# Optimization experiments

Measured on AMD Instinct MI355X. Metric: run time of the kernel, lower is better.

## Reference

```python
import jax, jax.numpy as jnp
import numpy as np

B, S, D = 2, 4096, 1024
H = 16
DK = D // H  # 64


def setup_inputs() -> dict:
    key = jax.random.key(0)
    ks = jax.random.split(key, 7)
    scale = 1.0 / np.sqrt(D)
    return {
        "Q": jax.random.normal(ks[0], (B, S, D), jnp.float32),
        "K": jax.random.normal(ks[1], (B, S, D), jnp.float32),
        "V": jax.random.normal(ks[2], (B, S, D), jnp.float32),
        "Wq": jax.random.normal(ks[3], (H * DK, D), jnp.float32) * scale,
        "Wk": jax.random.normal(ks[4], (H * DK, D), jnp.float32) * scale,
        "Wv": jax.random.normal(ks[5], (H * DK, D), jnp.float32) * scale,
        "Wo": jax.random.normal(ks[6], (D, H * DK), jnp.float32) * scale,
    }


def reference(Q, K, V, Wq, Wk, Wv, Wo):
    # Linear projections (bias=False): x @ W.T
    q = (Q @ Wq.T).reshape(B, S, H, DK)  # slicing [:, :, i*dk:(i+1)*dk] == head axis
    k = (K @ Wk.T).reshape(B, S, H, DK)
    v = (V @ Wv.T).reshape(B, S, H, DK)
    # scores: softmax(QK^T / sqrt(d_k)) per head, no mask
    scores = jnp.einsum("bshd,bthd->bhst", q, k) / jnp.sqrt(jnp.float32(DK))
    attn = jax.nn.softmax(scores, axis=-1)
    heads = jnp.einsum("bhst,bthd->bshd", attn, v)  # (B, S, H, DK)
    out = heads.reshape(B, S, H * DK) @ Wo.T  # concat heads then output proj
    return out
```

## Files before the change

### kernel.cpp

```cpp
#include <hip/hip_runtime.h>
#include <hip/hip_bf16.h>
#include <math.h>

#define B_NUM 2
#define S_LEN 4096
#define D_DIM 1024
#define H_NUM 16
#define DKH   64

typedef __attribute__((ext_vector_type(8))) short short8;
typedef __attribute__((ext_vector_type(4))) float f32x4;

__device__ __forceinline__ unsigned short f2bf(float f) {
    unsigned int u = __float_as_uint(f);
    u = (u + 0x7FFFu + ((u >> 16) & 1u)) >> 16;
    return (unsigned short)u;
}

__device__ __forceinline__ unsigned pk_bf16(float lo, float hi) {
    __hip_bfloat162 h = __float22bfloat162_rn(make_float2(lo, hi));
    unsigned u; __builtin_memcpy(&u, &h, 4); return u;
}

__device__ __forceinline__ void async_ld16(const unsigned short* g, unsigned short* l) {
    __builtin_amdgcn_global_load_lds(
        (const __attribute__((address_space(1))) unsigned int*)g,
        (__attribute__((address_space(3))) unsigned int*)l, 16, 0, 0);
}

__global__ __launch_bounds__(256) void f2b_3(
    const float* __restrict__ x0, const float* __restrict__ x1, const float* __restrict__ x2,
    unsigned short* __restrict__ y0, unsigned short* __restrict__ y1, unsigned short* __restrict__ y2)
{
    const float* xs[3] = { x0, x1, x2 };
    unsigned short* ys[3] = { y0, y1, y2 };
    const float* x = xs[blockIdx.y];
    unsigned short* y = ys[blockIdx.y];
    int i = (blockIdx.x * 256 + threadIdx.x) * 8;
    float4 a = *(const float4*)(x + i);
    float4 b = *(const float4*)(x + i + 4);
    unsigned t[4] = { pk_bf16(a.x, a.y), pk_bf16(a.z, a.w),
                      pk_bf16(b.x, b.y), pk_bf16(b.z, b.w) };
    *(uint4*)(y + i) = *(const uint4*)t;
}
__global__ __launch_bounds__(256) void f2b_4(
    const float* __restrict__ x0, const float* __restrict__ x1,
    const float* __restrict__ x2, const float* __restrict__ x3,
    unsigned short* __restrict__ y0, unsigned short* __restrict__ y1,
    unsigned short* __restrict__ y2, unsigned short* __restrict__ y3)
{
    const float* xs[4] = { x0, x1, x2, x3 };
    unsigned short* ys[4] = { y0, y1, y2, y3 };
    const float* x = xs[blockIdx.y];
    unsigned short* y = ys[blockIdx.y];
    int i = (blockIdx.x * 256 + threadIdx.x) * 8;
    float4 a = *(const float4*)(x + i);
    float4 b = *(const float4*)(x + i + 4);
    unsigned t[4] = { pk_bf16(a.x, a.y), pk_bf16(a.z, a.w),
                      pk_bf16(b.x, b.y), pk_bf16(b.z, b.w) };
    *(uint4*)(y + i) = *(const uint4*)t;
}

__device__ __forceinline__ void gemm_core(
    const unsigned short* __restrict__ A, const unsigned short* __restrict__ Wt,
    unsigned short* As, unsigned short* Bs,
    int m0, int n0, int K, f32x4 (&acc)[4][4])
{
    const int tid  = threadIdx.x;
    const int lane = tid & 63;
    const int wave = tid >> 6;
    const int quad = lane >> 4;
    const int l15  = lane & 15;
    const int wm = (wave >> 1) * 64;
    const int wn = (wave & 1) * 64;

    const int c0 = tid, c1 = tid + 256;
    const unsigned short* A0 = A  + (size_t)(m0 + (c0 >> 2)) * K + (c0 & 3) * 8;
    const unsigned short* A1 = A  + (size_t)(m0 + (c1 >> 2)) * K + (c1 & 3) * 8;
    const unsigned short* W0 = Wt + (size_t)(n0 + (c0 >> 2)) * K + (c0 & 3) * 8;
    const unsigned short* W1 = Wt + (size_t)(n0 + (c1 >> 2)) * K + (c1 & 3) * 8;

    for (int k0 = 0; k0 < K; k0 += 32) {
        __syncthreads();
        async_ld16(A0 + k0, &As[c0 * 8]);
        async_ld16(A1 + k0, &As[c1 * 8]);
        async_ld16(W0 + k0, &Bs[c0 * 8]);
        async_ld16(W1 + k0, &Bs[c1 * 8]);
        __syncthreads();

        short8 af[4], bfr[4];
        #pragma unroll
        for (int i = 0; i < 4; ++i)
            af[i] = *(const short8*)&As[(wm + i * 16 + l15) * 32 + quad * 8];
        #pragma unroll
        for (int j = 0; j < 4; ++j)
            bfr[j] = *(const short8*)&Bs[(wn + j * 16 + l15) * 32 + quad * 8];
        #pragma unroll
        for (int i = 0; i < 4; ++i)
            #pragma unroll
            for (int j = 0; j < 4; ++j)
                acc[i][j] = __builtin_amdgcn_mfma_f32_16x16x32_bf16(af[i], bfr[j], acc[i][j], 0, 0, 0);
    }
}

__global__ __launch_bounds__(256) void gemm_qkv(
    const unsigned short* __restrict__ Qb, const unsigned short* __restrict__ Kb,
    const unsigned short* __restrict__ Vb,
    const unsigned short* __restrict__ Wq, const unsigned short* __restrict__ Wk,
    const unsigned short* __restrict__ Wv,
    unsigned short* __restrict__ qo, unsigned short* __restrict__ ko,
    unsigned short* __restrict__ vto)
{
    __shared__ unsigned short As[128 * 32];
    __shared__ unsigned short Bs[128 * 32];

    const int z = blockIdx.z;
    const unsigned short* A  = (z == 0) ? Qb : (z == 1) ? Kb : Vb;
    const unsigned short* Wt = (z == 0) ? Wq : (z == 1) ? Wk : Wv;
    const float scale = (z == 0) ? 0.125f * 1.4426950408889634f : 1.0f;

    const int m0 = blockIdx.y * 128;
    const int n0 = blockIdx.x * 128;

    const f32x4 fzero = {0.f, 0.f, 0.f, 0.f};
    f32x4 acc[4][4];
    #pragma unroll
    for (int i = 0; i < 4; ++i)
        #pragma unroll
        for (int j = 0; j < 4; ++j) acc[i][j] = fzero;

    gemm_core(A, Wt, As, Bs, m0, n0, D_DIM, acc);

    const int lane = threadIdx.x & 63;
    const int wave = threadIdx.x >> 6;
    const int quad = lane >> 4;
    const int l15  = lane & 15;
    const int wm = (wave >> 1) * 64;
    const int wn = (wave & 1) * 64;

    if (z < 2) {
        unsigned short* out = (z == 0) ? qo : ko;
        #pragma unroll
        for (int i = 0; i < 4; ++i)
            #pragma unroll
            for (int j = 0; j < 4; ++j)
                #pragma unroll
                for (int r = 0; r < 4; ++r) {
                    const int row = m0 + wm + i * 16 + quad * 4 + r;
                    const int col = n0 + wn + j * 16 + l15;
                    out[(size_t)row * D_DIM + col] = f2bf(acc[i][j][r] * scale);
                }
    } else {
        #pragma unroll
        for (int i = 0; i < 4; ++i)
            #pragma unroll
            for (int j = 0; j < 4; ++j) {
                const int row = m0 + wm + i * 16 + quad * 4;
                const int col = n0 + wn + j * 16 + l15;
                const int bb = row >> 12, ss = row & (S_LEN - 1);
                uint2 u;
                u.x = pk_bf16(acc[i][j][0], acc[i][j][1]);
                u.y = pk_bf16(acc[i][j][2], acc[i][j][3]);
                *(uint2*)&vto[((size_t)(bb * H_NUM * DKH) + col) * S_LEN + ss] = u;
            }
    }
}

__global__ __launch_bounds__(256) void gemm_out(
    const unsigned short* __restrict__ A, const unsigned short* __restrict__ Wt,
    float* __restrict__ C)
{
    __shared__ unsigned short As[128 * 32];
    __shared__ unsigned short Bs[128 * 32];

    const int m0 = blockIdx.y * 128;
    const int n0 = blockIdx.x * 128;

    const f32x4 fzero = {0.f, 0.f, 0.f, 0.f};
    f32x4 acc[4][4];
    #pragma unroll
    for (int i = 0; i < 4; ++i)
        #pragma unroll
        for (int j = 0; j < 4; ++j) acc[i][j] = fzero;

    gemm_core(A, Wt, As, Bs, m0, n0, D_DIM, acc);

    const int lane = threadIdx.x & 63;
    const int wave = threadIdx.x >> 6;
    const int quad = lane >> 4;
    const int l15  = lane & 15;
    const int wm = (wave >> 1) * 64;
    const int wn = (wave & 1) * 64;

    #pragma unroll
    for (int i = 0; i < 4; ++i)
        #pragma unroll
        for (int j = 0; j < 4; ++j)
            #pragma unroll
            for (int r = 0; r < 4; ++r) {
                const int row = m0 + wm + i * 16 + quad * 4 + r;
                const int col = n0 + wn + j * 16 + l15;
                C[(size_t)row * D_DIM + col] = acc[i][j][r];
            }
}

__global__ __launch_bounds__(256, 2) void flash_mfma(
    const unsigned short* __restrict__ q, const unsigned short* __restrict__ k,
    const unsigned short* __restrict__ vt, unsigned short* __restrict__ hp)
{
    __shared__ unsigned short Ks[64 * 64];
    __shared__ unsigned short Vt[64 * 64];
    __shared__ unsigned short Ps[256 * 64];

    const int tid  = threadIdx.x;
    const int lane = tid & 63;
    const int wave = tid >> 6;
    const int quad = lane >> 4;
    const int l15  = lane & 15;

    const int bx   = blockIdx.x;
    const int xcd  = bx & 7, slot = bx >> 3;
    const int g    = xcd + 8 * (slot >> 4);
    const int s0   = (slot & 15) * 256;
    const int b    = g >> 4, h = g & 15;
    const size_t base = (size_t)b * (S_LEN * D_DIM) + (size_t)h * DKH;
    const size_t vtb  = (size_t)g * (DKH * S_LEN);

    short8 qf[4][2];
    #pragma unroll
    for (int nb = 0; nb < 4; ++nb)
        #pragma unroll
        for (int kk = 0; kk < 2; ++kk)
            qf[nb][kk] = *(const short8*)(q + base +
                (size_t)(s0 + wave * 64 + nb * 16 + l15) * D_DIM + kk * 32 + quad * 8);

    const f32x4 fzero = {0.f, 0.f, 0.f, 0.f};
    f32x4 o[4][4];
    float lacc[4] = {};
    #pragma unroll
    for (int i = 0; i < 4; ++i)
        #pragma unroll
        for (int j = 0; j < 4; ++j) o[i][j] = fzero;

    const int sr  = tid >> 3;
    const int sch = tid & 7;

    uint4 kpre[2], vpre[2];
    #pragma unroll
    for (int it = 0; it < 2; ++it) {
        const int r = sr + it * 32;
        kpre[it] = *(const uint4*)(k + base + (size_t)r * D_DIM + sch * 8);
        vpre[it] = *(const uint4*)(vt + vtb + (size_t)r * S_LEN + sch * 8);
    }

    for (int t0 = 0; t0 < S_LEN; t0 += 64) {
        __syncthreads();
        #pragma unroll
        for (int it = 0; it < 2; ++it) {
            const int r = sr + it * 32;
            *(uint4*)&Ks[r * 64 + ((sch ^ (r & 7)) << 3)] = kpre[it];
            *(uint4*)&Vt[r * 64 + ((sch ^ (r & 7)) << 3)] = vpre[it];
        }
        __syncthreads();
        if (t0 + 64 < S_LEN) {
            #pragma unroll
            for (int it = 0; it < 2; ++it) {
                const int r = sr + it * 32;
                kpre[it] = *(const uint4*)(k + base + (size_t)(t0 + 64 + r) * D_DIM + sch * 8);
                vpre[it] = *(const uint4*)(vt + vtb + (size_t)r * S_LEN + t0 + 64 + sch * 8);
            }
        }

        #pragma unroll
        for (int mh = 0; mh < 2; ++mh) {
            short8 kf[2][2];
            #pragma unroll
            for (int mi = 0; mi < 2; ++mi)
                #pragma unroll
                for (int kk = 0; kk < 2; ++kk) {
                    const int rr = (mh * 2 + mi) * 16 + l15;
                    kf[mi][kk] = *(const short8*)&Ks[rr * 64 + (((kk * 4 + quad) ^ (rr & 7)) << 3)];
                }
            f32x4 st[2][4];
            #pragma unroll
            for (int mi = 0; mi < 2; ++mi)
                #pragma unroll
                for (int nb = 0; nb < 4; ++nb) st[mi][nb] = fzero;
            #pragma unroll
            for (int kk = 0; kk < 2; ++kk)
                #pragma unroll
                for (int mi = 0; mi < 2; ++mi)
                    #pragma unroll
                    for (int nb = 0; nb < 4; ++nb)
                        st[mi][nb] = __builtin_amdgcn_mfma_f32_16x16x32_bf16(
                            kf[mi][kk], qf[nb][kk], st[mi][nb], 0, 0, 0);

            #pragma unroll
            for (int mi = 0; mi < 2; ++mi)
                #pragma unroll
                for (int nb = 0; nb < 4; ++nb) {
                    float p0 = __builtin_amdgcn_exp2f(st[mi][nb][0]);
                    float p1 = __builtin_amdgcn_exp2f(st[mi][nb][1]);
                    float p2 = __builtin_amdgcn_exp2f(st[mi][nb][2]);
                    float p3 = __builtin_amdgcn_exp2f(st[mi][nb][3]);
                    lacc[nb] += (p0 + p1) + (p2 + p3);
                    uint2 u;
                    u.x = pk_bf16(p0, p1);
                    u.y = pk_bf16(p2, p3);
                    const int row = wave * 64 + nb * 16 + l15;
                    const int c8  = (mh * 2 + mi) * 4 + quad;
                    *(uint2*)&Ps[row * 64 + ((c8 ^ (l15 & 14)) << 2)] = u;
                }
        }

        #pragma unroll
        for (int kk = 0; kk < 2; ++kk) {
            short8 vf[4], pf[4];
            #pragma unroll
            for (int mb = 0; mb < 4; ++mb) {
                const int rv = mb * 16 + l15;
                vf[mb] = *(const short8*)&Vt[rv * 64 + (((kk * 4 + quad) ^ (rv & 7)) << 3)];
            }
            #pragma unroll
            for (int nb = 0; nb < 4; ++nb) {
                const int rp = wave * 64 + nb * 16 + l15;
                pf[nb] = *(const short8*)&Ps[rp * 64 + (((kk * 8 + quad * 2) ^ (l15 & 14)) << 2)];
            }
            #pragma unroll
            for (int mb = 0; mb < 4; ++mb)
                #pragma unroll
                for (int nb = 0; nb < 4; ++nb)
                    o[mb][nb] = __builtin_amdgcn_mfma_f32_16x16x32_bf16(
                        vf[mb], pf[nb], o[mb][nb], 0, 0, 0);
        }
    }

    #pragma unroll
    for (int nb = 0; nb < 4; ++nb) {
        float l = lacc[nb];
        l += __shfl_xor(l, 16);
        l += __shfl_xor(l, 32);
        const float inv = 1.f / l;
        const int row = s0 + wave * 64 + nb * 16 + l15;
        #pragma unroll
        for (int mb = 0; mb < 4; ++mb) {
            uint2 u;
            u.x = pk_bf16(o[mb][nb][0] * inv, o[mb][nb][1] * inv);
            u.y = pk_bf16(o[mb][nb][2] * inv, o[mb][nb][3] * inv);
            *(uint2*)&hp[base + (size_t)row * D_DIM + mb * 16 + quad * 4] = u;
        }
    }
}

extern "C" void kernel_launch(void* const* d_in, const int* in_sizes, int n_in,
                              void* d_out, int out_size, void* d_ws, size_t ws_size,
                              hipStream_t stream) {
    const float* Q  = (const float*)d_in[0];
    const float* K  = (const float*)d_in[1];
    const float* V  = (const float*)d_in[2];
    const float* Wq = (const float*)d_in[3];
    const float* Wk = (const float*)d_in[4];
    const float* Wv = (const float*)d_in[5];
    const float* Wo = (const float*)d_in[6];

    const int NBSD = 8388608;
    const int NW   = 1048576;

    unsigned short* Qb  = (unsigned short*)d_ws;
    unsigned short* Kb  = Qb  + NBSD;
    unsigned short* Vb  = Kb  + NBSD;
    unsigned short* Wqb = Vb  + NBSD;
    unsigned short* Wkb = Wqb + NW;
    unsigned short* Wvb = Wkb + NW;
    unsigned short* Wob = Wvb + NW;
    unsigned short* qp  = Wob + NW;
    unsigned short* kp  = qp  + NBSD;
    unsigned short* vtp = kp  + NBSD;
    unsigned short* hb  = vtp + NBSD;

    f2b_3<<<dim3(NBSD / 2048, 3), 256, 0, stream>>>(Q, K, V, Qb, Kb, Vb);
    f2b_4<<<dim3(NW / 2048, 4), 256, 0, stream>>>(Wq, Wk, Wv, Wo, Wqb, Wkb, Wvb, Wob);

    const int M = B_NUM * S_LEN;
    dim3 gqkv(D_DIM / 128, M / 128, 3);
    gemm_qkv<<<gqkv, 256, 0, stream>>>(Qb, Kb, Vb, Wqb, Wkb, Wvb, qp, kp, vtp);

    flash_mfma<<<512, 256, 0, stream>>>(qp, kp, vtp, hb);

    gemm_out<<<dim3(D_DIM / 128, M / 128), 256, 0, stream>>>(hb, Wob, (float*)d_out);
}
```

Before: 464.4 us.

## Double-buffer K/V shared tiles and raise wave priority around MFMA blocks

Turns the K and Vt shared-memory tiles into two-stage ping-pong buffers. Each iteration stores the next tile into the idle buffer while computing on the current one, which cuts the two barriers per iteration to one. It also wraps the MFMA loops in s_setprio so waves issuing matrix instructions get scheduling priority over waves doing loads and exp. The cost is 16 KB of extra LDS per block, which may reduce occupancy at the requested 2 blocks per CU.

```diff
diff --git a/kernel.cpp b/kernel.cpp
--- a/kernel.cpp
+++ b/kernel.cpp
@@ -208,8 +208,8 @@
     const unsigned short* __restrict__ q, const unsigned short* __restrict__ k,
     const unsigned short* __restrict__ vt, unsigned short* __restrict__ hp)
 {
-    __shared__ unsigned short Ks[64 * 64];
-    __shared__ unsigned short Vt[64 * 64];
+    __shared__ unsigned short Ks[2][64 * 64];
+    __shared__ unsigned short Vt[2][64 * 64];
     __shared__ unsigned short Ps[256 * 64];
 
     const int tid  = threadIdx.x;
@@ -244,30 +244,43 @@
 
     const int sr  = tid >> 3;
     const int sch = tid & 7;
+    const int swz0 = ((sch ^ (sr & 7)) << 3);
+    const int swz1 = ((sch ^ ((sr + 32) & 7)) << 3);
 
     uint4 kpre[2], vpre[2];
-    #pragma unroll
-    for (int it = 0; it < 2; ++it) {
-        const int r = sr + it * 32;
-        kpre[it] = *(const uint4*)(k + base + (size_t)r * D_DIM + sch * 8);
-        vpre[it] = *(const uint4*)(vt + vtb + (size_t)r * S_LEN + sch * 8);
+    {
+        kpre[0] = *(const uint4*)(k + base + (size_t)sr * D_DIM + sch * 8);
+        kpre[1] = *(const uint4*)(k + base + (size_t)(sr + 32) * D_DIM + sch * 8);
+        vpre[0] = *(const uint4*)(vt + vtb + (size_t)sr * S_LEN + sch * 8);
+        vpre[1] = *(const uint4*)(vt + vtb + (size_t)(sr + 32) * S_LEN + sch * 8);
+        *(uint4*)&Ks[0][sr * 64 + swz0] = kpre[0];
+        *(uint4*)&Ks[0][(sr + 32) * 64 + swz1] = kpre[1];
+        *(uint4*)&Vt[0][sr * 64 + swz0] = vpre[0];
+        *(uint4*)&Vt[0][(sr + 32) * 64 + swz1] = vpre[1];
+        kpre[0] = *(const uint4*)(k + base + (size_t)(64 + sr) * D_DIM + sch * 8);
+        kpre[1] = *(const uint4*)(k + base + (size_t)(64 + sr + 32) * D_DIM + sch * 8);
+        vpre[0] = *(const uint4*)(vt + vtb + (size_t)sr * S_LEN + 64 + sch * 8);
+        vpre[1] = *(const uint4*)(vt + vtb + (size_t)(sr + 32) * S_LEN + 64 + sch * 8);
     }
+    __syncthreads();
 
     for (int t0 = 0; t0 < S_LEN; t0 += 64) {
-        __syncthreads();
-        #pragma unroll
-        for (int it = 0; it < 2; ++it) {
-            const int r = sr + it * 32;
-            *(uint4*)&Ks[r * 64 + ((sch ^ (r & 7)) << 3)] = kpre[it];
-            *(uint4*)&Vt[r * 64 + ((sch ^ (r & 7)) << 3)] = vpre[it];
-        }
-        __syncthreads();
+        const int cur = (t0 >> 6) & 1;
+        const unsigned short* Kc = Ks[cur];
+        const unsigned short* Vc = Vt[cur];
+
         if (t0 + 64 < S_LEN) {
-            #pragma unroll
-            for (int it = 0; it < 2; ++it) {
-                const int r = sr + it * 32;
-                kpre[it] = *(const uint4*)(k + base + (size_t)(t0 + 64 + r) * D_DIM + sch * 8);
-                vpre[it] = *(const uint4*)(vt + vtb + (size_t)r * S_LEN + t0 + 64 + sch * 8);
+            unsigned short* Kn = Ks[cur ^ 1];
+            unsigned short* Vn = Vt[cur ^ 1];
+            *(uint4*)&Kn[sr * 64 + swz0] = kpre[0];
+            *(uint4*)&Kn[(sr + 32) * 64 + swz1] = kpre[1];
+            *(uint4*)&Vn[sr * 64 + swz0] = vpre[0];
+            *(uint4*)&Vn[(sr + 32) * 64 + swz1] = vpre[1];
+            if (t0 + 128 < S_LEN) {
+                kpre[0] = *(const uint4*)(k + base + (size_t)(t0 + 128 + sr) * D_DIM + sch * 8);
+                kpre[1] = *(const uint4*)(k + base + (size_t)(t0 + 128 + sr + 32) * D_DIM + sch * 8);
+                vpre[0] = *(const uint4*)(vt + vtb + (size_t)sr * S_LEN + t0 + 128 + sch * 8);
+                vpre[1] = *(const uint4*)(vt + vtb + (size_t)(sr + 32) * S_LEN + t0 + 128 + sch * 8);
             }
         }
 
@@ -279,13 +292,14 @@
                 #pragma unroll
                 for (int kk = 0; kk < 2; ++kk) {
                     const int rr = (mh * 2 + mi) * 16 + l15;
-                    kf[mi][kk] = *(const short8*)&Ks[rr * 64 + (((kk * 4 + quad) ^ (rr & 7)) << 3)];
+                    kf[mi][kk] = *(const short8*)&Kc[rr * 64 + (((kk * 4 + quad) ^ (rr & 7)) << 3)];
                 }
             f32x4 st[2][4];
             #pragma unroll
             for (int mi = 0; mi < 2; ++mi)
                 #pragma unroll
                 for (int nb = 0; nb < 4; ++nb) st[mi][nb] = fzero;
+            __builtin_amdgcn_s_setprio(1);
             #pragma unroll
             for (int kk = 0; kk < 2; ++kk)
                 #pragma unroll
@@ -294,6 +308,7 @@
                     for (int nb = 0; nb < 4; ++nb)
                         st[mi][nb] = __builtin_amdgcn_mfma_f32_16x16x32_bf16(
                             kf[mi][kk], qf[nb][kk], st[mi][nb], 0, 0, 0);
+            __builtin_amdgcn_s_setprio(0);
 
             #pragma unroll
             for (int mi = 0; mi < 2; ++mi)
@@ -319,20 +334,24 @@
             #pragma unroll
             for (int mb = 0; mb < 4; ++mb) {
                 const int rv = mb * 16 + l15;
-                vf[mb] = *(const short8*)&Vt[rv * 64 + (((kk * 4 + quad) ^ (rv & 7)) << 3)];
+                vf[mb] = *(const short8*)&Vc[rv * 64 + (((kk * 4 + quad) ^ (rv & 7)) << 3)];
             }
             #pragma unroll
             for (int nb = 0; nb < 4; ++nb) {
                 const int rp = wave * 64 + nb * 16 + l15;
                 pf[nb] = *(const short8*)&Ps[rp * 64 + (((kk * 8 + quad * 2) ^ (l15 & 14)) << 2)];
             }
+            __builtin_amdgcn_s_setprio(1);
             #pragma unroll
             for (int mb = 0; mb < 4; ++mb)
                 #pragma unroll
                 for (int nb = 0; nb < 4; ++nb)
                     o[mb][nb] = __builtin_amdgcn_mfma_f32_16x16x32_bf16(
                         vf[mb], pf[nb], o[mb][nb], 0, 0, 0);
+            __builtin_amdgcn_s_setprio(0);
         }
+
+        __syncthreads();
     }
 
     #pragma unroll
```

Measured after the change: 445.0 us. 4.2% less time.
